# Optimization experiments

Hardware: AMD Instinct MI355X
Metric: run time of the kernel (lower is better)

Reference implementation:

```python
import jax, jax.numpy as jnp
import numpy as np


def setup_inputs() -> dict:
    key0 = jax.random.key(0)
    kq, kk, kv = jax.random.split(key0, 3)
    B, S, E = 4, 2048, 1024
    query = jax.random.normal(kq, (B, S, E), dtype=jnp.float32)
    key = jax.random.normal(kk, (B, S, E), dtype=jnp.float32)
    value = jax.random.normal(kv, (B, S, E), dtype=jnp.float32)
    attn_mask = jnp.zeros((B, S, S), dtype=jnp.float32)
    return {"query": query, "key": key, "value": value, "attn_mask": attn_mask}


def reference(query, key, value, attn_mask):
    # qk = Q K^T / sqrt(E) + mask; softmax over last dim; dropout is
    # identity in eval mode (reference baseline); out = attn @ V.
    E = query.shape[-1]
    scale = 1.0 / jnp.sqrt(jnp.asarray(E, dtype=query.dtype))
    qk = jnp.einsum("bqe,bke->bqk", query, key) * scale + attn_mask
    attn = jax.nn.softmax(qk, axis=-1)
    out = jnp.einsum("bqk,bke->bqe", attn, value)
    return out
```

## Files before the change

kernel.cpp:

```cpp
#include <hip/hip_runtime.h>
#include <stdint.h>
#include <math.h>

typedef unsigned short u16;
typedef short bf16x8 __attribute__((ext_vector_type(8)));
typedef unsigned short u16x8 __attribute__((ext_vector_type(8)));
typedef unsigned short u16x4 __attribute__((ext_vector_type(4)));
typedef float f32x4 __attribute__((ext_vector_type(4)));

typedef __attribute__((address_space(1))) const void gvoid;
typedef __attribute__((address_space(3))) void lvoid;

#define LOG2E 1.4426950408889634f

__device__ __forceinline__ float bf2f(u16 u) {
  union { unsigned int i; float f; } v; v.i = ((unsigned int)u) << 16; return v.f;
}
__device__ __forceinline__ u16 f2bf(float f) {
  union { float ff; unsigned int i; } v; v.ff = f;
  unsigned int x = v.i;
  return (u16)((x + 0x7FFFu + ((x >> 16) & 1u)) >> 16);
}

__global__ __launch_bounds__(256)
void cvt_f32_bf16(const float* __restrict__ src, u16* __restrict__ dst, long n)
{
  long i = ((long)blockIdx.x * 256 + threadIdx.x) * 8;
  if (i + 8 > n) return;
  f32x4 a = *(const f32x4*)&src[i];
  f32x4 b = *(const f32x4*)&src[i + 4];
  u16x8 o;
#pragma unroll
  for (int j = 0; j < 4; j++) { o[j] = f2bf(a[j]); o[4 + j] = f2bf(b[j]); }
  *(u16x8*)&dst[i] = o;
}

__global__ __launch_bounds__(256)
void transcvt_v(const float* __restrict__ V, u16* __restrict__ VT, int S, int E)
{
  __shared__ u16 t[64][72];
  const int b = blockIdx.z;
  const float* Vb = V + (long)b * S * E;
  u16* VTb = VT + (long)b * S * E;
  const int k0 = blockIdx.x * 64, n0 = blockIdx.y * 64;
  const int tid = threadIdx.x;
#pragma unroll
  for (int p = 0; p < 2; p++) {
    int kk = p * 32 + (tid >> 3);
    int nn = (tid & 7) * 8;
    f32x4 a = *(const f32x4*)&Vb[(long)(k0 + kk) * E + n0 + nn];
    f32x4 c = *(const f32x4*)&Vb[(long)(k0 + kk) * E + n0 + nn + 4];
#pragma unroll
    for (int j = 0; j < 4; j++) { t[nn + j][kk] = f2bf(a[j]); t[nn + 4 + j][kk] = f2bf(c[j]); }
  }
  __syncthreads();
#pragma unroll
  for (int p = 0; p < 2; p++) {
    int nn = p * 32 + (tid >> 3);
    int kk = (tid & 7) * 8;
    u16x8 u;
#pragma unroll
    for (int j = 0; j < 8; j++) u[j] = t[nn][kk + j];
    *(u16x8*)&VTb[(long)(n0 + nn) * S + k0 + kk] = u;
  }
}

template<int HASMASK, int COUT>
__global__ __launch_bounds__(256, 3)
void gemm_bt_fast(const u16* __restrict__ A, int lda, long aRowOff,
                  const u16* __restrict__ B, int ldb, long bBatchStride,
                  void* __restrict__ Cp, int ldc, long cRowOff,
                  const float* __restrict__ maskf,
                  int K, float scale, long g0, int S)
{
  const int tid  = threadIdx.x;
  const int lane = tid & 63;
  const int wave = tid >> 6;
  const long gTile = g0 + (long)blockIdx.y * 128;
  const int  bidx  = (int)(gTile / S);
  const int  nTile = blockIdx.x * 128;

  __shared__ u16 As[2][128][32];
  __shared__ u16 Bs[2][128][32];

  const u16* Ab = A + (gTile - aRowOff) * (long)lda;
  const u16* Bb = B + (long)bidx * bBatchStride + (long)nTile * ldb;

  const int qm = (wave >> 1) * 64;
  const int qn = (wave & 1) * 64;
  const int lm  = lane & 15;
  const int lk8 = (lane >> 4) * 8;

  const int sr = lane >> 2;
  const int sc = (lane & 3) * 8;

  f32x4 acc[4][4];
#pragma unroll
  for (int i = 0; i < 4; i++)
#pragma unroll
    for (int j = 0; j < 4; j++) acc[i][j] = (f32x4){0.f, 0.f, 0.f, 0.f};

  for (int k0 = 0; k0 < K; k0 += 64) {
#pragma unroll
    for (int p = 0; p < 4; p++) {
      const int c  = wave * 4 + p;
      const int j  = c >> 3;
      const int cl = c & 7;
      const int rr = cl * 16 + sr;
      const int gc = k0 + j * 32 + sc;
      __builtin_amdgcn_global_load_lds(
          (gvoid*)&Ab[(long)rr * lda + gc],
          (lvoid*)((char*)&As[0][0][0] + c * 1024),
          16, 0, 0);
      __builtin_amdgcn_global_load_lds(
          (gvoid*)&Bb[(long)rr * ldb + gc],
          (lvoid*)((char*)&Bs[0][0][0] + c * 1024),
          16, 0, 0);
    }
    __syncthreads();

#pragma unroll
    for (int s = 0; s < 2; s++) {
      bf16x8 af[4], bfr[4];
#pragma unroll
      for (int rt = 0; rt < 4; rt++)
        af[rt] = *(const bf16x8*)&As[s][qm + rt * 16 + lm][lk8];
#pragma unroll
      for (int ct = 0; ct < 4; ct++)
        bfr[ct] = *(const bf16x8*)&Bs[s][qn + ct * 16 + lm][lk8];
#pragma unroll
      for (int rt = 0; rt < 4; rt++)
#pragma unroll
        for (int ct = 0; ct < 4; ct++)
          acc[rt][ct] = __builtin_amdgcn_mfma_f32_16x16x32_bf16(af[rt], bfr[ct], acc[rt][ct], 0, 0, 0);
    }
    __syncthreads();
  }

  const int lr = (lane >> 4) * 4;
#pragma unroll
  for (int rt = 0; rt < 4; rt++) {
#pragma unroll
    for (int ct = 0; ct < 4; ct++) {
      long gr = gTile + qm + rt * 16 + lr;
      int  cc = nTile + qn + ct * 16 + lm;
#pragma unroll
      for (int i = 0; i < 4; i++) {
        float v = acc[rt][ct][i] * scale;
        if (HASMASK) v += maskf[(gr + i) * (long)ldc + cc];
        if (COUT == 0)
          ((u16*)Cp)[(gr + i - cRowOff) * (long)ldc + cc] = f2bf(v);
        else
          ((float*)Cp)[(gr + i - cRowOff) * (long)ldc + cc] = v;
      }
    }
  }
}

template<int ASRC, int BSRC, int BMODE, int HASMASK, int COUT>
__global__ __launch_bounds__(256, 2)
void gemm_bt(const void* __restrict__ Ap, int lda, long aRowOff,
             const void* __restrict__ Bp, int ldb, long bBatchStride,
             void* __restrict__ Cp, int ldc, long cRowOff,
             const float* __restrict__ maskf,
             int K, float scale, long g0, int S)
{
  const int tid  = threadIdx.x;
  const int lane = tid & 63;
  const int wave = tid >> 6;
  const long gTile = g0 + (long)blockIdx.y * 128;
  const int  b     = (int)(gTile / S);
  const int  nTile = blockIdx.x * 128;

  __shared__ u16 As[128][40];
  __shared__ u16 Bs[128][40];

  const int qm = (wave >> 1) * 64;
  const int qn = (wave & 1) * 64;

  f32x4 acc[4][4];
#pragma unroll
  for (int i = 0; i < 4; i++)
#pragma unroll
    for (int j = 0; j < 4; j++) acc[i][j] = (f32x4){0.f, 0.f, 0.f, 0.f};

  const u16*   Ab = (const u16*)Ap   + (gTile - aRowOff) * (long)lda;
  const float* Af = (const float*)Ap + (gTile - aRowOff) * (long)lda;
  const u16*   Bb = (const u16*)Bp   + (long)b * bBatchStride;
  const float* Bf = (const float*)Bp + (long)b * bBatchStride;

  const int lm = lane & 15;
  const int lk = (lane >> 4) * 8;

  for (int k0 = 0; k0 < K; k0 += 32) {
    if (ASRC == 0) {
      int srow = tid >> 2, scol = (tid & 3) * 8;
#pragma unroll
      for (int p = 0; p < 2; p++) {
        int r = p * 64 + srow;
        *(u16x8*)&As[r][scol] = *(const u16x8*)&Ab[(long)r * lda + k0 + scol];
      }
    } else {
      int srow = tid >> 3, scol = (tid & 7) * 4;
#pragma unroll
      for (int p = 0; p < 4; p++) {
        int r = p * 32 + srow;
        f32x4 a = *(const f32x4*)&Af[(long)r * lda + k0 + scol];
        u16x4 o;
#pragma unroll
        for (int j = 0; j < 4; j++) o[j] = f2bf(a[j]);
        *(u16x4*)&As[r][scol] = o;
      }
    }
    if (BMODE == 0) {
      if (BSRC == 0) {
        int srow = tid >> 2, scol = (tid & 3) * 8;
#pragma unroll
        for (int p = 0; p < 2; p++) {
          int r = p * 64 + srow;
          *(u16x8*)&Bs[r][scol] = *(const u16x8*)&Bb[(long)(nTile + r) * ldb + k0 + scol];
        }
      } else {
        int srow = tid >> 3, scol = (tid & 7) * 4;
#pragma unroll
        for (int p = 0; p < 4; p++) {
          int r = p * 32 + srow;
          f32x4 a = *(const f32x4*)&Bf[(long)(nTile + r) * ldb + k0 + scol];
          u16x4 o;
#pragma unroll
          for (int j = 0; j < 4; j++) o[j] = f2bf(a[j]);
          *(u16x4*)&Bs[r][scol] = o;
        }
      }
    }
    __syncthreads();

    bf16x8 af[4], bfr[4];
#pragma unroll
    for (int rt = 0; rt < 4; rt++)
      af[rt] = *(const bf16x8*)&As[qm + rt * 16 + lm][lk];
    if (BMODE == 0) {
#pragma unroll
      for (int ct = 0; ct < 4; ct++)
        bfr[ct] = *(const bf16x8*)&Bs[qn + ct * 16 + lm][lk];
    } else {
#pragma unroll
      for (int ct = 0; ct < 4; ct++) {
        const float* vp = Bf + (long)(k0 + lk) * ldb + nTile + qn + ct * 16 + lm;
#pragma unroll
        for (int j = 0; j < 8; j++) bfr[ct][j] = (short)f2bf(vp[(long)j * ldb]);
      }
    }
#pragma unroll
    for (int rt = 0; rt < 4; rt++)
#pragma unroll
      for (int ct = 0; ct < 4; ct++)
        acc[rt][ct] = __builtin_amdgcn_mfma_f32_16x16x32_bf16(af[rt], bfr[ct], acc[rt][ct], 0, 0, 0);
    __syncthreads();
  }

  const int lr = (lane >> 4) * 4;
#pragma unroll
  for (int rt = 0; rt < 4; rt++) {
#pragma unroll
    for (int ct = 0; ct < 4; ct++) {
      long gr = gTile + qm + rt * 16 + lr;
      int  cc = nTile + qn + ct * 16 + lm;
#pragma unroll
      for (int i = 0; i < 4; i++) {
        float v = acc[rt][ct][i] * scale;
        if (HASMASK) v += maskf[(gr + i) * (long)ldc + cc];
        if (COUT == 0)
          ((u16*)Cp)[(gr + i - cRowOff) * (long)ldc + cc] = f2bf(v);
        else
          ((float*)Cp)[(gr + i - cRowOff) * (long)ldc + cc] = v;
      }
    }
  }
}

__global__ __launch_bounds__(256)
void softmax_rows(u16* __restrict__ Sbuf, int ncols)
{
  const long row = blockIdx.x;
  u16* rp = Sbuf + row * (long)ncols;
  const int tid = threadIdx.x;

  u16x8 u = *(const u16x8*)&rp[tid * 8];
  float x[8];
  float m = -3.0e38f;
#pragma unroll
  for (int i = 0; i < 8; i++) { x[i] = bf2f(u[i]); m = fmaxf(m, x[i]); }
#pragma unroll
  for (int off = 32; off; off >>= 1) m = fmaxf(m, __shfl_xor(m, off, 64));
  __shared__ float redm[4];
  if ((tid & 63) == 0) redm[tid >> 6] = m;
  __syncthreads();
  m = fmaxf(fmaxf(redm[0], redm[1]), fmaxf(redm[2], redm[3]));

  float e[8];
  float s = 0.f;
#pragma unroll
  for (int i = 0; i < 8; i++) { e[i] = exp2f((x[i] - m) * LOG2E); s += e[i]; }
#pragma unroll
  for (int off = 32; off; off >>= 1) s += __shfl_xor(s, off, 64);
  __shared__ float reds[4];
  if ((tid & 63) == 0) reds[tid >> 6] = s;
  __syncthreads();
  s = reds[0] + reds[1] + reds[2] + reds[3];

  float inv = 1.0f / s;
  u16x8 o;
#pragma unroll
  for (int i = 0; i < 8; i++) o[i] = f2bf(e[i] * inv);
  *(u16x8*)&rp[tid * 8] = o;
}

extern "C" void kernel_launch(void* const* d_in, const int* in_sizes, int n_in,
                              void* d_out, int out_size, void* d_ws, size_t ws_size,
                              hipStream_t stream)
{
  const float* Q    = (const float*)d_in[0];
  const float* Km   = (const float*)d_in[1];
  const float* V    = (const float*)d_in[2];
  const float* mask = (const float*)d_in[3];
  float* out = (float*)d_out;

  const long qsz = in_sizes[0];
  const long msz = in_sizes[3];
  const long E = 1024;
  const long S = (msz / qsz) * E;
  const long B = qsz / (S * E);
  const long G = B * S;
  const float scale = 1.0f / sqrtf((float)E);

  const size_t convBytes = (size_t)(3 * qsz) * 2;
  const size_t rowBytes  = (size_t)S * 2;
  char* w = (char*)d_ws;
  size_t avail = ws_size;
  const bool haveConv = (ws_size >= convBytes + 128 * rowBytes);

  u16 *Qb = nullptr, *Kb = nullptr, *VTb = nullptr;
  if (haveConv) {
    Qb  = (u16*)w;              w += (size_t)qsz * 2;
    Kb  = (u16*)w;              w += (size_t)qsz * 2;
    VTb = (u16*)w;              w += (size_t)qsz * 2;
    avail -= convBytes;
  }
  long Rmax = (long)((avail / rowBytes) / 128) * 128;
  if (Rmax > G) Rmax = G;
  if (Rmax < 128) Rmax = 128;
  u16* Sbuf = (u16*)w;

  if (haveConv) {
    cvt_f32_bf16<<<dim3((unsigned)(qsz / 2048)), 256, 0, stream>>>(Q, Qb, qsz);
    cvt_f32_bf16<<<dim3((unsigned)(qsz / 2048)), 256, 0, stream>>>(Km, Kb, qsz);
    transcvt_v<<<dim3(S / 64, E / 64, B), 256, 0, stream>>>(V, VTb, (int)S, (int)E);
  }

  for (long g0 = 0; g0 < G; g0 += Rmax) {
    const long R = (G - g0 < Rmax) ? (G - g0) : Rmax;
    if (haveConv) {
      gemm_bt_fast<1, 0><<<dim3(S / 128, R / 128), 256, 0, stream>>>(
          Qb, (int)E, 0L, Kb, (int)E, S * E,
          Sbuf, (int)S, g0, mask, (int)E, scale, g0, (int)S);
    } else {
      gemm_bt<1, 1, 0, 1, 0><<<dim3(S / 128, R / 128), 256, 0, stream>>>(
          Q, (int)E, 0L, Km, (int)E, S * E,
          Sbuf, (int)S, g0, mask, (int)E, scale, g0, (int)S);
    }
    softmax_rows<<<dim3(R), 256, 0, stream>>>(Sbuf, (int)S);
    if (haveConv) {
      gemm_bt_fast<0, 1><<<dim3(E / 128, R / 128), 256, 0, stream>>>(
          Sbuf, (int)S, g0, VTb, (int)S, E * S,
          out, (int)E, 0L, nullptr, (int)S, 1.0f, g0, (int)S);
    } else {
      gemm_bt<0, 1, 1, 0, 1><<<dim3(E / 128, R / 128), 256, 0, stream>>>(
          Sbuf, (int)S, g0, V, (int)E, S * E,
          out, (int)E, 0L, nullptr, (int)S, 1.0f, g0, (int)S);
    }
  }
}
```

Baseline: 289.6 us.

## Double-buffer GEMM K-loop with 32-wide stages to overlap loads and MFMA

Restructures the GEMM main loop from a single-buffered 64-wide K step, which needed two barriers per iteration, into a double-buffered 32-wide K pipeline. The global-to-LDS async loads for the next tile are issued before computing the current buffer, and only one barrier is used per step. The goal is to hide global load latency behind the MFMA work. In exchange there are twice as many loop iterations with half the compute per barrier. The change also assumes K is a multiple of 32.

```diff
diff --git a/kernel.cpp b/kernel.cpp
--- a/kernel.cpp
+++ b/kernel.cpp
@@ -100,42 +100,49 @@
 #pragma unroll
     for (int j = 0; j < 4; j++) acc[i][j] = (f32x4){0.f, 0.f, 0.f, 0.f};
 
-  for (int k0 = 0; k0 < K; k0 += 64) {
-#pragma unroll
-    for (int p = 0; p < 4; p++) {
-      const int c  = wave * 4 + p;
-      const int j  = c >> 3;
-      const int cl = c & 7;
-      const int rr = cl * 16 + sr;
-      const int gc = k0 + j * 32 + sc;
+  auto STAGE = [&](int buf, int t) {
+#pragma unroll
+    for (int p = 0; p < 2; p++) {
+      const int chunk = wave * 2 + p;
+      const int rr = chunk * 16 + sr;
+      const int gc = t * 32 + sc;
       __builtin_amdgcn_global_load_lds(
           (gvoid*)&Ab[(long)rr * lda + gc],
-          (lvoid*)((char*)&As[0][0][0] + c * 1024),
+          (lvoid*)((char*)&As[buf][0][0] + chunk * 1024),
           16, 0, 0);
       __builtin_amdgcn_global_load_lds(
           (gvoid*)&Bb[(long)rr * ldb + gc],
-          (lvoid*)((char*)&Bs[0][0][0] + c * 1024),
+          (lvoid*)((char*)&Bs[buf][0][0] + chunk * 1024),
           16, 0, 0);
     }
+  };
+
+  auto COMPUTE = [&](int buf) {
+    bf16x8 af[4], bfr[4];
+#pragma unroll
+    for (int rt = 0; rt < 4; rt++)
+      af[rt] = *(const bf16x8*)&As[buf][qm + rt * 16 + lm][lk8];
+#pragma unroll
+    for (int ct = 0; ct < 4; ct++)
+      bfr[ct] = *(const bf16x8*)&Bs[buf][qn + ct * 16 + lm][lk8];
+#pragma unroll
+    for (int rt = 0; rt < 4; rt++)
+#pragma unroll
+      for (int ct = 0; ct < 4; ct++)
+        acc[rt][ct] = __builtin_amdgcn_mfma_f32_16x16x32_bf16(af[rt], bfr[ct], acc[rt][ct], 0, 0, 0);
+  };
+
+  const int nt = K >> 5;
+  STAGE(0, 0);
+  __syncthreads();
+  int cur = 0;
+  for (int t = 0; t < nt - 1; t++) {
+    STAGE(cur ^ 1, t + 1);
+    COMPUTE(cur);
     __syncthreads();
-
-#pragma unroll
-    for (int s = 0; s < 2; s++) {
-      bf16x8 af[4], bfr[4];
-#pragma unroll
-      for (int rt = 0; rt < 4; rt++)
-        af[rt] = *(const bf16x8*)&As[s][qm + rt * 16 + lm][lk8];
-#pragma unroll
-      for (int ct = 0; ct < 4; ct++)
-        bfr[ct] = *(const bf16x8*)&Bs[s][qn + ct * 16 + lm][lk8];
-#pragma unroll
-      for (int rt = 0; rt < 4; rt++)
-#pragma unroll
-        for (int ct = 0; ct < 4; ct++)
-          acc[rt][ct] = __builtin_amdgcn_mfma_f32_16x16x32_bf16(af[rt], bfr[ct], acc[rt][ct], 0, 0, 0);
-    }
-    __syncthreads();
-  }
+    cur ^= 1;
+  }
+  COMPUTE(cur);
 
   const int lr = (lane >> 4) * 4;
 #pragma unroll
```

Measured after the change: 297.5 us. +2.7%, slower.
